# Kernel tuning notes

Hardware: AMD Instinct MI355X
Metric: run time of the kernel (lower is better)

Reference implementation:

```python
import jax, jax.numpy as jnp
import numpy as np

MAX_NORM = 1.0
B, V, C, VOCAB, E = 256, 50, 32, 100000, 128


def setup_inputs() -> dict:
    key = jax.random.key(0)
    k1, k2, k3 = jax.random.split(key, 3)
    W = jax.random.normal(k1, (VOCAB, E), dtype=jnp.float32)
    codes = jax.random.randint(k2, (B, V, C), 0, VOCAB, dtype=jnp.int64)
    n_visits = jax.random.randint(k3, (B,), 1, V + 1, dtype=jnp.int64)
    # ensure batch_max_visits == V (static output shape, matches min(max(len), max_visits))
    n_visits = n_visits.at[0].set(V)
    return {"W": W, "codes": codes, "n_visits": n_visits}


def reference(W, codes, n_visits):
    # Faithful to the torch module: expand_visits produces offsets [0,1,...,nv-1],
    # so EmbeddingBag('sum') bag i = emb(flat[i]) for i < nv-1, and the last bag
    # sums emb(flat[nv-1 : nv*C]). Result is top-padded to V rows per patient.
    b, v, c = codes.shape
    L = v * c
    flat = codes.reshape(b, L)                     # flattened codes per patient
    g = W[flat]                                    # [B, L, E] gathered rows
    # EmbeddingBag max_norm: renormalize looked-up rows whose norm exceeds MAX_NORM
    norms = jnp.linalg.norm(g, axis=-1, keepdims=True)
    g = g * jnp.minimum(1.0, MAX_NORM / jnp.maximum(norms, 1e-12))
    # prefix sums: cs0[:, j] = sum of g[:, :j]
    cs0 = jnp.concatenate([jnp.zeros((b, 1, g.shape[-1]), g.dtype),
                           jnp.cumsum(g, axis=1)], axis=1)  # [B, L+1, E]
    nv = n_visits.astype(jnp.int32)                # [B]
    end = (nv * c)[:, None, None]                  # sum over real flattened codes
    start = (nv - 1)[:, None, None]
    S = (jnp.take_along_axis(cs0, end, axis=1)
         - jnp.take_along_axis(cs0, start, axis=1))  # [B, 1, E] last-bag sum
    r = jnp.arange(v, dtype=jnp.int32)[None, :]    # output row index
    i = r - (v - nv[:, None])                      # bag index (negative => pad row)
    ei = jnp.take_along_axis(g, jnp.clip(i, 0, L - 1)[:, :, None], axis=1)  # [B, V, E]
    out = jnp.where((i >= 0)[:, :, None],
                    jnp.where((i < nv[:, None] - 1)[:, :, None], ei, S),
                    jnp.zeros_like(ei))
    return out
```

## Files before the change

### kernel.cpp

```cpp
#include <hip/hip_runtime.h>
#include <math.h>

#define B_     256
#define V_     50
#define C_     32
#define E_     128
#define VOCAB_ 100000
#define L_     (V_ * C_)
#define SPB    8
#define NCHUNK (SPB * 4)
#define NBLK   (B_ * SPB)


__device__ __forceinline__ float dot8(const float4 v1, const float4 v2) {
    return v1.x*v1.x + v1.y*v1.y + v1.z*v1.z + v1.w*v1.w
         + v2.x*v2.x + v2.y*v2.y + v2.z*v2.z + v2.w*v2.w;
}

__global__ __launch_bounds__(256, 4) void fused_kernel(
    const float* __restrict__ W,
    const int*   __restrict__ codes,
    const int*   __restrict__ nvis,
    float*       __restrict__ out,
    float*       __restrict__ part)
{
    const int tid  = threadIdx.x;
    const int wave = tid >> 6;
    const int lane = tid & 63;
    const int g    = lane >> 4;
    const int l4   = lane & 15;

    const int b  = blockIdx.x >> 3;
    const int s  = blockIdx.x & (SPB - 1);
    const int nv = nvis[b];
    const int* cf = codes + b * L_;
    float* ob = out + (size_t)b * V_ * E_;

    const int j0    = nv - 1;
    const int j1    = nv * C_;
    const int chunk = (j1 - j0 + NCHUNK - 1) / NCHUNK;
    const int wid   = s * 4 + wave;
    const int a0    = j0 + wid * chunk;
    const int n     = min(a0 + chunk, j1) - a0;
    int cl = 0;
    if (lane < n) cl = cf[a0 + lane];

    {
        const int i = (wave * 4 + g) * SPB + s;
        if (i < V_ - 1) {
            if (i < nv - 1) {
                const int code = cf[i];
                const float* row = W + (size_t)code * E_;
                float4 v1 = ((const float4*)row)[l4];
                float4 v2 = ((const float4*)row)[16 + l4];
                float ss = dot8(v1, v2);
                #pragma unroll
                for (int m = 1; m <= 8; m <<= 1) ss += __shfl_xor(ss, m, 64);
                const float sc = fminf(1.0f, 1.0f / fmaxf(sqrtf(ss), 1e-12f));
                float* orow = ob + (size_t)(V_ - nv + i) * E_;
                ((float4*)orow)[l4]      = make_float4(v1.x*sc, v1.y*sc, v1.z*sc, v1.w*sc);
                ((float4*)orow)[16 + l4] = make_float4(v2.x*sc, v2.y*sc, v2.z*sc, v2.w*sc);
            } else {
                float* orow = ob + (size_t)(i - (nv - 1)) * E_;
                ((float4*)orow)[l4]      = make_float4(0.f, 0.f, 0.f, 0.f);
                ((float4*)orow)[16 + l4] = make_float4(0.f, 0.f, 0.f, 0.f);
            }
        }
    }

    float4 a1 = make_float4(0.f, 0.f, 0.f, 0.f);
    float4 a2 = make_float4(0.f, 0.f, 0.f, 0.f);

#define ISSUE(T, XV1, XV2, YV1, YV2) do {                                   \
        const int cA = __shfl(cl, (T) + g, 64);                             \
        const int cB = __shfl(cl, (T) + 4 + g, 64);                         \
        const float4* rA = (const float4*)(W + (size_t)cA * E_);            \
        const float4* rB = (const float4*)(W + (size_t)cB * E_);            \
        XV1 = rA[l4]; XV2 = rA[16 + l4];                                    \
        YV1 = rB[l4]; YV2 = rB[16 + l4];                                    \
    } while (0)

#define PROC(T, XV1, XV2, YV1, YV2) do {                                    \
        float ssA = dot8(XV1, XV2);                                         \
        float ssB = dot8(YV1, YV2);                                         \
        _Pragma("unroll")                                                   \
        for (int m = 1; m <= 8; m <<= 1) {                                  \
            ssA += __shfl_xor(ssA, m, 64);                                  \
            ssB += __shfl_xor(ssB, m, 64);                                  \
        }                                                                   \
        float scA = fminf(1.0f, 1.0f / fmaxf(sqrtf(ssA), 1e-12f));          \
        float scB = fminf(1.0f, 1.0f / fmaxf(sqrtf(ssB), 1e-12f));          \
        if ((T) + g     >= n) scA = 0.0f;                                   \
        if ((T) + 4 + g >= n) scB = 0.0f;                                   \
        a1.x += XV1.x*scA + YV1.x*scB; a1.y += XV1.y*scA + YV1.y*scB;       \
        a1.z += XV1.z*scA + YV1.z*scB; a1.w += XV1.w*scA + YV1.w*scB;       \
        a2.x += XV2.x*scA + YV2.x*scB; a2.y += XV2.y*scA + YV2.y*scB;       \
        a2.z += XV2.z*scA + YV2.z*scB; a2.w += XV2.w*scA + YV2.w*scB;       \
    } while (0)

    if (n > 0) {
        float4 Av1, Av2, Bv1, Bv2;
        float4 Cv1, Cv2, Dv1, Dv2;
        ISSUE(0, Av1, Av2, Bv1, Bv2);
        int t = 0;
        for (; t + 8 < n; t += 8) {
            ISSUE(t + 8, Cv1, Cv2, Dv1, Dv2);
            PROC(t, Av1, Av2, Bv1, Bv2);
            Av1 = Cv1; Av2 = Cv2; Bv1 = Dv1; Bv2 = Dv2;
        }
        PROC(t, Av1, Av2, Bv1, Bv2);
    }
#undef ISSUE
#undef PROC

    #pragma unroll
    for (int m = 16; m <= 32; m <<= 1) {
        a1.x += __shfl_xor(a1.x, m, 64); a1.y += __shfl_xor(a1.y, m, 64);
        a1.z += __shfl_xor(a1.z, m, 64); a1.w += __shfl_xor(a1.w, m, 64);
        a2.x += __shfl_xor(a2.x, m, 64); a2.y += __shfl_xor(a2.y, m, 64);
        a2.z += __shfl_xor(a2.z, m, 64); a2.w += __shfl_xor(a2.w, m, 64);
    }

    __shared__ float4 s1[4][16], s2[4][16];
    if (lane < 16) { s1[wave][l4] = a1; s2[wave][l4] = a2; }
    __syncthreads();
    if (tid < 32) {
        const int h = tid >> 4;
        const int q = tid & 15;
        float4 f = (h == 0) ? s1[0][q] : s2[0][q];
        #pragma unroll
        for (int w = 1; w < 4; w++) {
            float4 p = (h == 0) ? s1[w][q] : s2[w][q];
            f.x += p.x; f.y += p.y; f.z += p.z; f.w += p.w;
        }
        ((float4*)(part + (size_t)blockIdx.x * E_))[tid] = f;
    }
}

__global__ __launch_bounds__(128) void reduce_kernel(
    const float* __restrict__ part,
    float*       __restrict__ out)
{
    const int b = blockIdx.x;
    const int t = threadIdx.x;
    const float* p = part + (size_t)b * SPB * E_;
    float acc = 0.0f;
    #pragma unroll
    for (int s = 0; s < SPB; s++) acc += p[s * E_ + t];
    out[((size_t)b * V_ + (V_ - 1)) * E_ + t] = acc;
}

extern "C" void kernel_launch(void* const* d_in, const int* in_sizes, int n_in,
                              void* d_out, int out_size, void* d_ws, size_t ws_size,
                              hipStream_t stream) {
    const float* W     = (const float*)d_in[0];
    const int*   codes = (const int*)d_in[1];
    const int*   nvis  = (const int*)d_in[2];
    float*       out   = (float*)d_out;
    float*       part  = (float*)d_ws;

    fused_kernel<<<NBLK, 256, 0, stream>>>(W, codes, nvis, out, part);
    reduce_kernel<<<B_, 128, 0, stream>>>(part, out);
}
```

Baseline: 97.57 us.

## Use one 1024-thread block per patient with LDS-staged codes, drop reduce kernel

Moves from eight 256-thread blocks per patient plus a separate reduction kernel to a single 16-wave block per patient. The patient's codes are staged in shared memory, and the last-bag sum is reduced across waves in LDS and written directly to the output. This removes the partial-sum workspace round-trip and a second kernel launch. In exchange it cuts the grid to 256 blocks, which lowers the number of waves in flight to hide gather latency. It also ties the runtime to the largest patient, since one patient's work can no longer spread across several CUs.

```diff
diff --git a/kernel.cpp b/kernel.cpp
--- a/kernel.cpp
+++ b/kernel.cpp
@@ -7,9 +7,8 @@
 #define E_     128
 #define VOCAB_ 100000
 #define L_     (V_ * C_)
-#define SPB    8
-#define NCHUNK (SPB * 4)
-#define NBLK   (B_ * SPB)
+#define NW     16
+#define THREADS (NW * 64)
 
 
 __device__ __forceinline__ float dot8(const float4 v1, const float4 v2) {
@@ -17,39 +16,38 @@
          + v2.x*v2.x + v2.y*v2.y + v2.z*v2.z + v2.w*v2.w;
 }
 
-__global__ __launch_bounds__(256, 4) void fused_kernel(
+__global__ __launch_bounds__(THREADS, 4) void fused_kernel(
     const float* __restrict__ W,
     const int*   __restrict__ codes,
     const int*   __restrict__ nvis,
-    float*       __restrict__ out,
-    float*       __restrict__ part)
+    float*       __restrict__ out)
 {
+    __shared__ int    scode[L_ + 16];
+    __shared__ float4 s1[NW][16], s2[NW][16];
+
     const int tid  = threadIdx.x;
     const int wave = tid >> 6;
     const int lane = tid & 63;
     const int g    = lane >> 4;
     const int l4   = lane & 15;
 
-    const int b  = blockIdx.x >> 3;
-    const int s  = blockIdx.x & (SPB - 1);
+    const int b  = blockIdx.x;
     const int nv = nvis[b];
     const int* cf = codes + b * L_;
     float* ob = out + (size_t)b * V_ * E_;
 
-    const int j0    = nv - 1;
-    const int j1    = nv * C_;
-    const int chunk = (j1 - j0 + NCHUNK - 1) / NCHUNK;
-    const int wid   = s * 4 + wave;
-    const int a0    = j0 + wid * chunk;
-    const int n     = min(a0 + chunk, j1) - a0;
-    int cl = 0;
-    if (lane < n) cl = cf[a0 + lane];
+    const int j0 = nv - 1;
+    const int j1 = nv * C_;
+
+    for (int k = tid; k < j1; k += THREADS) scode[k] = cf[k];
+    if (tid < 16) scode[j1 + tid] = 0;
+    __syncthreads();
 
     {
-        const int i = (wave * 4 + g) * SPB + s;
+        const int i = wave * 4 + g;
         if (i < V_ - 1) {
             if (i < nv - 1) {
-                const int code = cf[i];
+                const int code = scode[i];
                 const float* row = W + (size_t)code * E_;
                 float4 v1 = ((const float4*)row)[l4];
                 float4 v2 = ((const float4*)row)[16 + l4];
@@ -68,12 +66,16 @@
         }
     }
 
+    const int chunk = (j1 - j0 + NW - 1) / NW;
+    const int a0    = j0 + wave * chunk;
+    const int n     = min(a0 + chunk, j1) - a0;
+
     float4 a1 = make_float4(0.f, 0.f, 0.f, 0.f);
     float4 a2 = make_float4(0.f, 0.f, 0.f, 0.f);
 
 #define ISSUE(T, XV1, XV2, YV1, YV2) do {                                   \
-        const int cA = __shfl(cl, (T) + g, 64);                             \
-        const int cB = __shfl(cl, (T) + 4 + g, 64);                         \
+        const int cA = scode[a0 + (T) + g];                                 \
+        const int cB = scode[a0 + (T) + 4 + g];                             \
         const float4* rA = (const float4*)(W + (size_t)cA * E_);            \
         const float4* rB = (const float4*)(W + (size_t)cB * E_);            \
         XV1 = rA[l4]; XV2 = rA[16 + l4];                                    \
@@ -121,33 +123,21 @@
         a2.z += __shfl_xor(a2.z, m, 64); a2.w += __shfl_xor(a2.w, m, 64);
     }
 
-    __shared__ float4 s1[4][16], s2[4][16];
     if (lane < 16) { s1[wave][l4] = a1; s2[wave][l4] = a2; }
     __syncthreads();
+
     if (tid < 32) {
         const int h = tid >> 4;
         const int q = tid & 15;
         float4 f = (h == 0) ? s1[0][q] : s2[0][q];
         #pragma unroll
-        for (int w = 1; w < 4; w++) {
+        for (int w = 1; w < NW; w++) {
             float4 p = (h == 0) ? s1[w][q] : s2[w][q];
             f.x += p.x; f.y += p.y; f.z += p.z; f.w += p.w;
         }
-        ((float4*)(part + (size_t)blockIdx.x * E_))[tid] = f;
+        float* orow = ob + (size_t)(V_ - 1) * E_;
+        ((float4*)orow)[tid] = f;
     }
-}
-
-__global__ __launch_bounds__(128) void reduce_kernel(
-    const float* __restrict__ part,
-    float*       __restrict__ out)
-{
-    const int b = blockIdx.x;
-    const int t = threadIdx.x;
-    const float* p = part + (size_t)b * SPB * E_;
-    float acc = 0.0f;
-    #pragma unroll
-    for (int s = 0; s < SPB; s++) acc += p[s * E_ + t];
-    out[((size_t)b * V_ + (V_ - 1)) * E_ + t] = acc;
 }
 
 extern "C" void kernel_launch(void* const* d_in, const int* in_sizes, int n_in,
@@ -157,8 +147,7 @@
     const int*   codes = (const int*)d_in[1];
     const int*   nvis  = (const int*)d_in[2];
     float*       out   = (float*)d_out;
-    float*       part  = (float*)d_ws;
+    (void)d_ws; (void)ws_size;
 
-    fused_kernel<<<NBLK, 256, 0, stream>>>(W, codes, nvis, out, part);
-    reduce_kernel<<<B_, 128, 0, stream>>>(part, out);
+    fused_kernel<<<B_, THREADS, 0, stream>>>(W, codes, nvis, out);
 }
```

New measurement: 97.42 us. About the same (-0.1%).
